# Optimization experiments

Hardware: AMD Instinct MI355X
Metric: run time of the kernel (lower is better)

Reference implementation:

```python
import jax, jax.numpy as jnp
import numpy as np

N = 50000       # nodes
E = 1_600_000   # edges (avg degree 32)
IN = 256        # in_dim
HID = 64        # hidden_dim
HEADS = 2
CLS = 10
NEG_SLOPE = 0.2  # PyG GATConv default leaky_relu slope


def gat_layer(x, edge_index, W, att_src, att_dst, bias, heads, concat):
    """PyG-style GATConv (eval mode, add_self_loops=True).
    x: [N, F_in]; W: [F_in, heads*C]; att_src/att_dst: [heads, C]; bias: [heads*C] or [C].
    """
    n = x.shape[0]
    loop = jnp.arange(n)
    src = jnp.concatenate([edge_index[0], loop])   # message sources j
    dst = jnp.concatenate([edge_index[1], loop])   # message targets i
    C = W.shape[1] // heads
    h = (x @ W).reshape(n, heads, C)               # [N, H, C]
    a_s = jnp.sum(h * att_src, axis=-1)            # [N, H]
    a_d = jnp.sum(h * att_dst, axis=-1)            # [N, H]
    e = jax.nn.leaky_relu(a_s[src] + a_d[dst], NEG_SLOPE)   # [E', H]
    # segment softmax over incoming edges of each destination node
    m = jax.lax.stop_gradient(jax.ops.segment_max(e, dst, num_segments=n))
    ex = jnp.exp(e - m[dst])
    denom = jax.ops.segment_sum(ex, dst, num_segments=n)
    alpha = ex / denom[dst]                         # [E', H]
    out = jax.ops.segment_sum(alpha[:, :, None] * h[src], dst, num_segments=n)  # [N, H, C]
    out = out.reshape(n, heads * C) if concat else out.mean(axis=1)
    return out + bias


def setup_inputs() -> dict:
    key = jax.random.key(0)
    ks = jax.random.split(key, 12)
    sd = lambda f: np.float32(1.0 / np.sqrt(f))
    x = jax.random.normal(ks[0], (N, IN), dtype=jnp.float32)
    edge_index = jax.random.randint(ks[1], (2, E), 0, N, dtype=jnp.int64)
    # layer 1: in_dim -> hidden, heads=2, concat
    W1 = jax.random.normal(ks[2], (IN, HEADS * HID), dtype=jnp.float32) * sd(IN)
    as1 = jax.random.normal(ks[3], (HEADS, HID), dtype=jnp.float32) * sd(HID)
    ad1 = jax.random.normal(ks[4], (HEADS, HID), dtype=jnp.float32) * sd(HID)
    b1 = jnp.zeros((HEADS * HID,), dtype=jnp.float32)
    # layer 2: hidden*heads -> hidden, heads=1, concat=False
    W2 = jax.random.normal(ks[5], (HEADS * HID, HID), dtype=jnp.float32) * sd(HEADS * HID)
    as2 = jax.random.normal(ks[6], (1, HID), dtype=jnp.float32) * sd(HID)
    ad2 = jax.random.normal(ks[7], (1, HID), dtype=jnp.float32) * sd(HID)
    b2 = jnp.zeros((HID,), dtype=jnp.float32)
    # linear head
    Wl = jax.random.normal(ks[8], (HID, CLS), dtype=jnp.float32) * sd(HID)
    bl = jnp.zeros((CLS,), dtype=jnp.float32)
    return {"x": x, "edge_index": edge_index,
            "W1": W1, "as1": as1, "ad1": ad1, "b1": b1,
            "W2": W2, "as2": as2, "ad2": ad2, "b2": b2,
            "Wl": Wl, "bl": bl}


def reference(x, edge_index, W1, as1, ad1, b1, W2, as2, ad2, b2, Wl, bl):
    h = jax.nn.elu(gat_layer(x, edge_index, W1, as1, ad1, b1, HEADS, True))
    h = jax.nn.elu(gat_layer(h, edge_index, W2, as2, ad2, b2, 1, False))
    return h @ Wl + bl  # [N, num_classes]
```

## Files before the change

kernel.cpp:

```cpp
#include <hip/hip_runtime.h>

#define NN 50000
#define NE 1600000
#define EP (NE + NN)
#define IN_DIM 256
#define HIDD 64
#define NCLS 10
#define NBKT 196
#define EPB 8192
#define NPB ((EP + EPB - 1) / EPB)
#define BCAP 12288

typedef unsigned short u16;
typedef short bf16x8 __attribute__((ext_vector_type(8)));
typedef float f32x4 __attribute__((ext_vector_type(4)));

__device__ __forceinline__ float b2f(u16 v) { return __uint_as_float(((unsigned)v) << 16); }
__device__ __forceinline__ u16 f2b(float f) {
    unsigned u = __float_as_uint(f);
    unsigned r = (u + 0x7FFFu + ((u >> 16) & 1u)) >> 16;
    return (u16)r;
}

__device__ __forceinline__ void load_edge(const int* __restrict__ ei, int m, int g,
                                          int& s, int& d) {
    if (g < NE) {
        if (m) { s = ei[2 * (size_t)g]; d = ei[2 * ((size_t)NE + g)]; }
        else   { s = ei[g];             d = ei[NE + g]; }
    } else {
        s = d = g - NE;
    }
    s = s < 0 ? 0 : (s >= NN ? NN - 1 : s);
    d = d < 0 ? 0 : (d >= NN ? NN - 1 : d);
}

__device__ __forceinline__ void wcvt_att_job(
    const float* __restrict__ W, const float* __restrict__ as,
    const float* __restrict__ ad, int K, int N, int H, u16* __restrict__ Wt,
    int idx) {
    if (idx >= K * (N + 16)) return;
    int n = idx / K, k = idx - n * K;
    if (n < N) { Wt[idx] = f2b(W[(size_t)k * N + n]); return; }
    int j = n - N;
    if (j >= 2 * H) { Wt[idx] = 0; return; }
    const float* att = (j & 1) ? ad : as;
    int h = j >> 1, C = N / H;
    float sum = 0.f;
    for (int c = 0; c < C; ++c)
        sum += W[(size_t)k * N + h * C + c] * att[h * C + c];
    Wt[idx] = f2b(sum);
}

__global__ __launch_bounds__(256) void setup_k(
    const int* __restrict__ ei, int* __restrict__ mode, int* __restrict__ gcursor,
    const float* __restrict__ W1, const float* __restrict__ as1,
    const float* __restrict__ ad1, u16* __restrict__ w1t,
    const float* __restrict__ W2, const float* __restrict__ as2,
    const float* __restrict__ ad2, u16* __restrict__ w2t) {
    int b = blockIdx.x, t = threadIdx.x;
    if (b == 0) {
        for (int i = t; i < NBKT; i += 256) gcursor[i] = 0;
        if (t < 64) {
            int nz = 0;
#pragma unroll
            for (int k = 0; k < 4; ++k) {
                int i = t * 4 + k;
                if (ei[2 * i + 1] != 0) nz = 1;
            }
            unsigned long long bal = __ballot(nz);
            if (t == 0) *mode = (bal == 0ULL) ? 1 : 0;
        }
    } else if (b <= 144) {
        wcvt_att_job(W1, as1, ad1, 256, 128, 2, w1t, (b - 1) * 256 + t);
    } else {
        wcvt_att_job(W2, as2, ad2, 128, 64, 1, w2t, (b - 145) * 256 + t);
    }
}

__global__ __launch_bounds__(256) void partition_k(const int* __restrict__ ei,
                                                   const int* __restrict__ mode,
                                                   int* __restrict__ gcursor,
                                                   unsigned* __restrict__ bbuf) {
    __shared__ int hist[NBKT], base[NBKT], cur[NBKT];
    __shared__ unsigned stash[EPB];
    int t = threadIdx.x;
    for (int i = t; i < NBKT; i += 256) hist[i] = 0;
    __syncthreads();
    int m = *mode;
    int g0 = blockIdx.x * EPB;
    int gend = min(g0 + EPB, EP);
    for (int g = g0 + t; g < gend; g += 256) {
        int s, d;
        load_edge(ei, m, g, s, d);
        stash[g - g0] = ((unsigned)s << 16) | (unsigned)d;
        atomicAdd(&hist[d >> 8], 1);
    }
    __syncthreads();
    for (int i = t; i < NBKT; i += 256) {
        base[i] = hist[i] ? atomicAdd(&gcursor[i], hist[i]) : 0;
        cur[i] = 0;
    }
    __syncthreads();
    int cnt = gend - g0;
    for (int l = t; l < cnt; l += 256) {
        unsigned p = stash[l];
        int d = p & 0xFFFF;
        int b = d >> 8;
        int r = base[b] + atomicAdd(&cur[b], 1);
        if (r < BCAP)
            bbuf[(size_t)b * BCAP + r] = ((p >> 16) << 8) | (unsigned)(d & 255);
    }
}

__global__ __launch_bounds__(256) void bucket_csr_k(const unsigned* __restrict__ bbuf,
                                                    const int* __restrict__ gcursor,
                                                    int* __restrict__ row_ptr,
                                                    u16* __restrict__ csr_src) {
    __shared__ int bsc[256];
    __shared__ int hist[256], scn[256], cur[256];
    __shared__ int se0, scnt, stot;
    int b = blockIdx.x, t = threadIdx.x;
    int v = (t < NBKT) ? min(gcursor[t], BCAP) : 0;
    bsc[t] = v;
    __syncthreads();
    for (int off = 1; off < 256; off <<= 1) {
        int x = (t >= off) ? bsc[t - off] : 0;
        __syncthreads();
        bsc[t] += x;
        __syncthreads();
    }
    if (t == b) { se0 = bsc[t] - v; scnt = v; }
    if (t == NBKT - 1) stot = bsc[t];
    hist[t] = 0;
    __syncthreads();
    int e0 = se0, cnt = scnt;
    const unsigned* bb = bbuf + (size_t)b * BCAP;
    for (int e = t; e < cnt; e += 256)
        atomicAdd(&hist[bb[e] & 255], 1);
    __syncthreads();
    int hv = hist[t];
    scn[t] = hv;
    __syncthreads();
    for (int off = 1; off < 256; off <<= 1) {
        int x = (t >= off) ? scn[t - off] : 0;
        __syncthreads();
        scn[t] += x;
        __syncthreads();
    }
    int ex = scn[t] - hv;
    int n = b * 256 + t;
    if (n < NN) row_ptr[n] = e0 + ex;
    cur[t] = e0 + ex;
    __syncthreads();
    for (int e = t; e < cnt; e += 256) {
        unsigned p = bb[e];
        int pos = atomicAdd(&cur[p & 255], 1);
        csr_src[pos] = (u16)(p >> 8);
    }
    if (b == 0 && t == 0) row_ptr[NN] = stot;
}

template <int K, int NF, int H, bool F32A>
__global__ __launch_bounds__(256) void gemm_mfma_att_k(
    const float* __restrict__ Af, const u16* __restrict__ Ab,
    const u16* __restrict__ Wt, u16* __restrict__ C,
    float* __restrict__ a_s, float* __restrict__ a_d) {
    constexpr int NTF = NF / 16, NT = NTF + 1, KS = K / 32;
    const int wave = threadIdx.x >> 6, lane = threadIdx.x & 63;
    const int quad = lane >> 4, l15 = lane & 15;
    const int m0 = blockIdx.x * 64 + wave * 16;
    int rowA = m0 + l15;
    if (rowA >= NN) rowA = NN - 1;
    const float* afp = F32A ? (Af + (size_t)rowA * K + quad * 8) : nullptr;
    const u16*   abp = F32A ? nullptr : (Ab + (size_t)rowA * K + quad * 8);
    const u16* bptr = Wt + (size_t)l15 * K + quad * 8;
    f32x4 acc[NT] = {};
#pragma unroll
    for (int ks = 0; ks < KS; ++ks) {
        bf16x8 af;
        if (F32A) {
            float4 v0 = *(const float4*)(afp + ks * 32);
            float4 v1 = *(const float4*)(afp + ks * 32 + 4);
            af[0] = (short)f2b(v0.x); af[1] = (short)f2b(v0.y);
            af[2] = (short)f2b(v0.z); af[3] = (short)f2b(v0.w);
            af[4] = (short)f2b(v1.x); af[5] = (short)f2b(v1.y);
            af[6] = (short)f2b(v1.z); af[7] = (short)f2b(v1.w);
        } else {
            af = *(const bf16x8*)(abp + ks * 32);
        }
        bf16x8 bf[NT];
#pragma unroll
        for (int nt = 0; nt < NT; ++nt)
            bf[nt] = *(const bf16x8*)(bptr + (size_t)nt * 16 * K + ks * 32);
#pragma unroll
        for (int nt = 0; nt < NT; ++nt)
            acc[nt] = __builtin_amdgcn_mfma_f32_16x16x32_bf16(af, bf[nt], acc[nt], 0, 0, 0);
    }
#pragma unroll
    for (int nt = 0; nt < NTF; ++nt) {
#pragma unroll
        for (int reg = 0; reg < 4; ++reg) {
            int row = m0 + quad * 4 + reg;
            if (row < NN) C[(size_t)row * NF + nt * 16 + l15] = f2b(acc[nt][reg]);
        }
    }
    if (l15 < 2 * H) {
        int h = l15 >> 1;
        float* dst = (l15 & 1) ? a_d : a_s;
#pragma unroll
        for (int reg = 0; reg < 4; ++reg) {
            int row = m0 + quad * 4 + reg;
            if (row < NN) dst[row * H + h] = acc[NTF][reg];
        }
    }
}

template <int CH, int H, bool HEAD>
__global__ __launch_bounds__(256) void gat_gather_k(
    const int* __restrict__ row_ptr, const u16* __restrict__ csr_src,
    const float* __restrict__ a_s, const float* __restrict__ a_d,
    const u16* __restrict__ h, const float* __restrict__ bias,
    u16* __restrict__ outg, const float* __restrict__ Wl,
    const float* __restrict__ bl, float* __restrict__ outh) {
    constexpr int VEC = CH / 64;
    constexpr int JB = 8;
    int n = (blockIdx.x * blockDim.x + threadIdx.x) >> 6;
    int lane = threadIdx.x & 63;
    if (n >= NN) return;
    int r0 = row_ptr[n], r1 = row_ptr[n + 1];
    const bool hi = (VEC == 2) ? (lane >= 32) : false;
    const u16* hlane = h + lane * VEC;

    float adn0, adn1 = 0.f;
    if (H == 2) {
        float2 adv = *(const float2*)(a_d + n * 2);
        adn0 = adv.x; adn1 = adv.y;
    } else {
        adn0 = a_d[n];
    }

    float dh0 = 0.f, dh1 = 0.f;
    float acc[VEC];
#pragma unroll
    for (int v = 0; v < VEC; ++v) acc[v] = 0.f;

    for (int base = r0; base < r1; base += 64) {
        int cnt = min(64, r1 - base);
        int idx = base + lane;
        bool act = idx < r1;
        int sl = act ? (int)csr_src[idx] : 0;
        unsigned pex;
        if (H == 2) {
            float2 av = *(const float2*)(a_s + sl * 2);
            float e0 = av.x + adn0;
            e0 = e0 > 0.f ? e0 : 0.2f * e0;
            e0 = fminf(e0, 60.f);
            float ex0 = act ? __expf(e0) : 0.f;
            dh0 += ex0;
            float e1 = av.y + adn1;
            e1 = e1 > 0.f ? e1 : 0.2f * e1;
            e1 = fminf(e1, 60.f);
            float ex1 = act ? __expf(e1) : 0.f;
            dh1 += ex1;
            pex = (unsigned)f2b(ex0) | ((unsigned)f2b(ex1) << 16);
        } else {
            float e0 = a_s[sl] + adn0;
            e0 = e0 > 0.f ? e0 : 0.2f * e0;
            e0 = fminf(e0, 60.f);
            float ex0 = act ? __expf(e0) : 0.f;
            dh0 += ex0;
            pex = (unsigned)sl | ((unsigned)f2b(ex0) << 16);
        }
        for (int j0 = 0; j0 < cnt; j0 += JB) {
            if (VEC == 2) {
                int ss[JB];
                unsigned pe[JB];
#pragma unroll
                for (int i = 0; i < JB; ++i) {
                    int j = j0 + i;
                    ss[i] = __shfl(sl, j);
                    pe[i] = (unsigned)__shfl((int)pex, j);
                }
                unsigned hv[JB];
#pragma unroll
                for (int i = 0; i < JB; ++i)
                    hv[i] = *(const unsigned*)(hlane + (size_t)ss[i] * CH);
#pragma unroll
                for (int i = 0; i < JB; ++i) {
                    float exv = hi ? __uint_as_float(pe[i] & 0xFFFF0000u)
                                   : __uint_as_float(pe[i] << 16);
                    acc[0] += exv * __uint_as_float(hv[i] << 16);
                    acc[1] += exv * __uint_as_float(hv[i] & 0xFFFF0000u);
                }
            } else {
                unsigned pe[JB];
#pragma unroll
                for (int i = 0; i < JB; ++i)
                    pe[i] = (unsigned)__shfl((int)pex, j0 + i);
                u16 hv[JB];
#pragma unroll
                for (int i = 0; i < JB; ++i)
                    hv[i] = hlane[(size_t)(pe[i] & 0xFFFFu) * CH];
#pragma unroll
                for (int i = 0; i < JB; ++i)
                    acc[0] += __uint_as_float(pe[i] & 0xFFFF0000u) * b2f(hv[i]);
            }
        }
    }

#pragma unroll
    for (int off = 32; off; off >>= 1) dh0 += __shfl_xor(dh0, off);
    float dn = dh0;
    if (H == 2) {
#pragma unroll
        for (int off = 32; off; off >>= 1) dh1 += __shfl_xor(dh1, off);
        dn = hi ? dh1 : dh0;
    }

    if (VEC == 2) {
        int c = lane * 2;
        float2 bv = *(const float2*)(bias + c);
        float v0 = acc[0] / dn + bv.x;
        float v1 = acc[1] / dn + bv.y;
        v0 = v0 > 0.f ? v0 : expm1f(v0);
        v1 = v1 > 0.f ? v1 : expm1f(v1);
        ushort2 ov;
        ov.x = f2b(v0); ov.y = f2b(v1);
        *(ushort2*)(outg + (size_t)n * CH + c) = ov;
    } else {
        float v0 = acc[0] / dn + bias[lane];
        v0 = v0 > 0.f ? v0 : expm1f(v0);
        if (HEAD) {
#pragma unroll
            for (int cls = 0; cls < NCLS; ++cls) {
                float p = v0 * Wl[lane * NCLS + cls];
#pragma unroll
                for (int off = 32; off; off >>= 1) p += __shfl_xor(p, off);
                if (lane == cls) outh[(size_t)n * NCLS + cls] = p + bl[cls];
            }
        } else {
            outg[(size_t)n * CH + lane] = f2b(v0);
        }
    }
}

extern "C" void kernel_launch(void* const* d_in, const int* in_sizes, int n_in,
                              void* d_out, int out_size, void* d_ws, size_t ws_size,
                              hipStream_t stream) {
    const float* x   = (const float*)d_in[0];
    const int*   ei  = (const int*)d_in[1];
    const float* W1  = (const float*)d_in[2];
    const float* as1 = (const float*)d_in[3];
    const float* ad1 = (const float*)d_in[4];
    const float* b1  = (const float*)d_in[5];
    const float* W2  = (const float*)d_in[6];
    const float* as2 = (const float*)d_in[7];
    const float* ad2 = (const float*)d_in[8];
    const float* b2  = (const float*)d_in[9];
    const float* Wl  = (const float*)d_in[10];
    const float* bl  = (const float*)d_in[11];
    float* out = (float*)d_out;

    float* ws = (float*)d_ws;
    size_t o = 0;
    u16* hb  = (u16*)(ws + o); o += (size_t)NN * 64;
    u16* g1  = (u16*)(ws + o); o += (size_t)NN * 64;
    unsigned* bbuf = (unsigned*)g1;
    u16* w1t = (u16*)(ws + o); o += 144 * 256 / 2;
    u16* w2t = (u16*)(ws + o); o += 80 * 128 / 2;
    float* a_s = ws + o;       o += (size_t)NN * 2;
    float* a_d = ws + o;       o += (size_t)NN * 2;
    int* ints = (int*)(ws + o);
    size_t io = 0;
    int* gcursor  = ints + io; io += NBKT;
    int* row_ptr  = ints + io; io += NN + 1;
    u16* csr_src  = (u16*)(ints + io); io += (EP + 1) / 2;
    int* mode     = ints + io; io += 1;

    setup_k<<<185, 256, 0, stream>>>(ei, mode, gcursor,
                                     W1, as1, ad1, w1t, W2, as2, ad2, w2t);

    partition_k<<<NPB, 256, 0, stream>>>(ei, mode, gcursor, bbuf);
    bucket_csr_k<<<NBKT, 256, 0, stream>>>(bbuf, gcursor, row_ptr, csr_src);

    const int gatherBlocks = (NN + 3) / 4;
    const int gemmBlocks = (NN + 63) / 64;

    gemm_mfma_att_k<256, 128, 2, true><<<gemmBlocks, 256, 0, stream>>>(
        x, nullptr, w1t, hb, a_s, a_d);
    gat_gather_k<128, 2, false><<<gatherBlocks, 256, 0, stream>>>(
        row_ptr, csr_src, a_s, a_d, hb, b1, g1, nullptr, nullptr, nullptr);

    gemm_mfma_att_k<128, 64, 1, false><<<gemmBlocks, 256, 0, stream>>>(
        nullptr, g1, w2t, hb, a_s, a_d);
    gat_gather_k<64, 1, true><<<gatherBlocks, 256, 0, stream>>>(
        row_ptr, csr_src, a_s, a_d, hb, b2, nullptr, Wl, bl, out);
}
```

Measured before the change: 324.6 us.

## Fold setup kernel into partition and use readlane broadcasts in gather

The separate setup kernel is removed. Weight conversion and attention-vector folding now run inside the first partition blocks, each block computes the int64/int32 mode flag into shared memory, and the bucket cursors are zeroed with a memset. This drops one kernel launch and its dependency gap. In the gather loop, cross-lane shuffles are replaced by readlane scalar broadcasts, and the per-lane exp selection becomes a shift, which should lower the VALU/LDS cost per edge. NPB is about 202, so it covers the 184 conversion blocks, but each block now also does the mode ballot, which adds a small amount of redundant work.

```diff
diff --git a/kernel.cpp b/kernel.cpp
--- a/kernel.cpp
+++ b/kernel.cpp
@@ -51,43 +51,31 @@
     Wt[idx] = f2b(sum);
 }
 
-__global__ __launch_bounds__(256) void setup_k(
-    const int* __restrict__ ei, int* __restrict__ mode, int* __restrict__ gcursor,
+__global__ __launch_bounds__(256) void partition_k(
+    const int* __restrict__ ei, int* __restrict__ gcursor,
+    unsigned* __restrict__ bbuf,
     const float* __restrict__ W1, const float* __restrict__ as1,
     const float* __restrict__ ad1, u16* __restrict__ w1t,
     const float* __restrict__ W2, const float* __restrict__ as2,
     const float* __restrict__ ad2, u16* __restrict__ w2t) {
-    int b = blockIdx.x, t = threadIdx.x;
-    if (b == 0) {
-        for (int i = t; i < NBKT; i += 256) gcursor[i] = 0;
-        if (t < 64) {
-            int nz = 0;
-#pragma unroll
-            for (int k = 0; k < 4; ++k) {
-                int i = t * 4 + k;
-                if (ei[2 * i + 1] != 0) nz = 1;
-            }
-            unsigned long long bal = __ballot(nz);
-            if (t == 0) *mode = (bal == 0ULL) ? 1 : 0;
-        }
-    } else if (b <= 144) {
-        wcvt_att_job(W1, as1, ad1, 256, 128, 2, w1t, (b - 1) * 256 + t);
-    } else {
-        wcvt_att_job(W2, as2, ad2, 128, 64, 1, w2t, (b - 145) * 256 + t);
-    }
-}
-
-__global__ __launch_bounds__(256) void partition_k(const int* __restrict__ ei,
-                                                   const int* __restrict__ mode,
-                                                   int* __restrict__ gcursor,
-                                                   unsigned* __restrict__ bbuf) {
     __shared__ int hist[NBKT], base[NBKT], cur[NBKT];
     __shared__ unsigned stash[EPB];
-    int t = threadIdx.x;
+    __shared__ int smode;
+    int t = threadIdx.x, b = blockIdx.x;
+    if (b < 144) wcvt_att_job(W1, as1, ad1, 256, 128, 2, w1t, b * 256 + t);
+    else if (b < 184) wcvt_att_job(W2, as2, ad2, 128, 64, 1, w2t, (b - 144) * 256 + t);
+    if (t < 64) {
+        int nz = 0;
+#pragma unroll
+        for (int k = 0; k < 4; ++k)
+            if (ei[2 * (t * 4 + k) + 1] != 0) nz = 1;
+        unsigned long long bal = __ballot(nz);
+        if (t == 0) smode = (bal == 0ULL) ? 1 : 0;
+    }
     for (int i = t; i < NBKT; i += 256) hist[i] = 0;
     __syncthreads();
-    int m = *mode;
-    int g0 = blockIdx.x * EPB;
+    int m = smode;
+    int g0 = b * EPB;
     int gend = min(g0 + EPB, EP);
     for (int g = g0 + t; g < gend; g += 256) {
         int s, d;
@@ -105,10 +93,10 @@
     for (int l = t; l < cnt; l += 256) {
         unsigned p = stash[l];
         int d = p & 0xFFFF;
-        int b = d >> 8;
-        int r = base[b] + atomicAdd(&cur[b], 1);
+        int bb = d >> 8;
+        int r = base[bb] + atomicAdd(&cur[bb], 1);
         if (r < BCAP)
-            bbuf[(size_t)b * BCAP + r] = ((p >> 16) << 8) | (unsigned)(d & 255);
+            bbuf[(size_t)bb * BCAP + r] = ((p >> 16) << 8) | (unsigned)(d & 255);
     }
 }
 
@@ -229,7 +217,7 @@
     if (n >= NN) return;
     int r0 = row_ptr[n], r1 = row_ptr[n + 1];
     const bool hi = (VEC == 2) ? (lane >= 32) : false;
-    const u16* hlane = h + lane * VEC;
+    const int shl16 = hi ? 0 : 16;
 
     float adn0, adn1 = 0.f;
     if (H == 2) {
@@ -273,37 +261,35 @@
         }
         for (int j0 = 0; j0 < cnt; j0 += JB) {
             if (VEC == 2) {
-                int ss[JB];
-                unsigned pe[JB];
+                int ssu[JB];
+                unsigned peu[JB];
 #pragma unroll
                 for (int i = 0; i < JB; ++i) {
-                    int j = j0 + i;
-                    ss[i] = __shfl(sl, j);
-                    pe[i] = (unsigned)__shfl((int)pex, j);
+                    ssu[i] = __builtin_amdgcn_readlane(sl, j0 + i);
+                    peu[i] = (unsigned)__builtin_amdgcn_readlane((int)pex, j0 + i);
                 }
                 unsigned hv[JB];
 #pragma unroll
                 for (int i = 0; i < JB; ++i)
-                    hv[i] = *(const unsigned*)(hlane + (size_t)ss[i] * CH);
+                    hv[i] = ((const unsigned*)(h + (size_t)ssu[i] * CH))[lane];
 #pragma unroll
                 for (int i = 0; i < JB; ++i) {
-                    float exv = hi ? __uint_as_float(pe[i] & 0xFFFF0000u)
-                                   : __uint_as_float(pe[i] << 16);
+                    float exv = __uint_as_float((peu[i] << shl16) & 0xFFFF0000u);
                     acc[0] += exv * __uint_as_float(hv[i] << 16);
                     acc[1] += exv * __uint_as_float(hv[i] & 0xFFFF0000u);
                 }
             } else {
-                unsigned pe[JB];
+                unsigned peu[JB];
 #pragma unroll
                 for (int i = 0; i < JB; ++i)
-                    pe[i] = (unsigned)__shfl((int)pex, j0 + i);
+                    peu[i] = (unsigned)__builtin_amdgcn_readlane((int)pex, j0 + i);
                 u16 hv[JB];
 #pragma unroll
                 for (int i = 0; i < JB; ++i)
-                    hv[i] = hlane[(size_t)(pe[i] & 0xFFFFu) * CH];
+                    hv[i] = (h + (size_t)(peu[i] & 0xFFFFu) * CH)[lane];
 #pragma unroll
                 for (int i = 0; i < JB; ++i)
-                    acc[0] += __uint_as_float(pe[i] & 0xFFFF0000u) * b2f(hv[i]);
+                    acc[0] += __uint_as_float(peu[i] & 0xFFFF0000u) * b2f(hv[i]);
             }
         }
     }
@@ -375,12 +361,10 @@
     int* gcursor  = ints + io; io += NBKT;
     int* row_ptr  = ints + io; io += NN + 1;
     u16* csr_src  = (u16*)(ints + io); io += (EP + 1) / 2;
-    int* mode     = ints + io; io += 1;
-
-    setup_k<<<185, 256, 0, stream>>>(ei, mode, gcursor,
-                                     W1, as1, ad1, w1t, W2, as2, ad2, w2t);
-
-    partition_k<<<NPB, 256, 0, stream>>>(ei, mode, gcursor, bbuf);
+
+    hipMemsetAsync(gcursor, 0, NBKT * sizeof(int), stream);
+    partition_k<<<NPB, 256, 0, stream>>>(ei, gcursor, bbuf,
+                                         W1, as1, ad1, w1t, W2, as2, ad2, w2t);
     bucket_csr_k<<<NBKT, 256, 0, stream>>>(bbuf, gcursor, row_ptr, csr_src);
 
     const int gatherBlocks = (NN + 3) / 4;
```

Measured after the change: 326.2 us. Within noise of the previous version (+0.5%).
